# Performance work log

Measured on AMD Instinct MI355X. Metric: run time of the kernel, lower is better.

The kernel has to match this reference:

```python
import jax, jax.numpy as jnp
import numpy as np

N_NODES = 50000
N_EDGES = 800000
IN_CH = 128
H1, C1 = 2, 64            # gat1: heads=2, out=64 -> concat 128
H2, C2 = 1, 32            # gat2: heads=1, out=out_channels=32, concat=False
NEG_SLOPE = 0.2           # PyG GATConv default negative_slope


def setup_inputs() -> dict:
    key = jax.random.key(0)
    ks = jax.random.split(key, 12)
    s = 0.05
    return {
        "x": jax.random.normal(ks[0], (N_NODES, IN_CH), dtype=jnp.float32),
        "edge_index": jax.random.randint(ks[1], (2, N_EDGES), 0, N_NODES, dtype=jnp.int64),
        # layer 1 params
        "W1": jax.random.normal(ks[2], (IN_CH, H1 * C1), dtype=jnp.float32) * s,
        "a1_src": jax.random.normal(ks[3], (H1, C1), dtype=jnp.float32) * s,
        "a1_dst": jax.random.normal(ks[4], (H1, C1), dtype=jnp.float32) * s,
        "b1": jax.random.normal(ks[5], (H1 * C1,), dtype=jnp.float32) * s,
        # layer 2 params
        "W2": jax.random.normal(ks[6], (H1 * C1, H2 * C2), dtype=jnp.float32) * s,
        "a2_src": jax.random.normal(ks[7], (H2, C2), dtype=jnp.float32) * s,
        "a2_dst": jax.random.normal(ks[8], (H2, C2), dtype=jnp.float32) * s,
        "b2": jax.random.normal(ks[9], (C2,), dtype=jnp.float32) * s,
    }


def _gat_conv(x, src, dst, W, a_src, a_dst, b, heads, out_ch, concat):
    """PyG GATConv (eval mode, self-loops already in src/dst)."""
    n = x.shape[0]
    h = (x @ W).reshape(n, heads, out_ch)               # [N,H,C]
    s_src = jnp.sum(h * a_src, axis=-1)                  # [N,H]
    s_dst = jnp.sum(h * a_dst, axis=-1)                  # [N,H]
    e = jax.nn.leaky_relu(s_src[src] + s_dst[dst], NEG_SLOPE)   # [E,H]
    # segment softmax over incoming edges of each destination node
    emax = jax.ops.segment_max(e, dst, num_segments=n)   # [N,H]
    emax = jax.lax.stop_gradient(emax)
    ee = jnp.exp(e - emax[dst])
    den = jax.ops.segment_sum(ee, dst, num_segments=n)   # [N,H]
    alpha = ee / den[dst]                                # [E,H]
    out = jax.ops.segment_sum(h[src] * alpha[..., None], dst, num_segments=n)  # [N,H,C]
    out = out.reshape(n, heads * out_ch) if concat else out.mean(axis=1)
    return out + b


def reference(x, edge_index, W1, a1_src, a1_dst, b1, W2, a2_src, a2_dst, b2):
    n = x.shape[0]
    loops = jnp.arange(n, dtype=edge_index.dtype)
    src = jnp.concatenate([edge_index[0], loops])
    dst = jnp.concatenate([edge_index[1], loops])
    h = _gat_conv(x, src, dst, W1, a1_src, a1_dst, b1, H1, C1, concat=True)
    h = jax.nn.elu(h)
    out = _gat_conv(h, src, dst, W2, a2_src, a2_dst, b2, H2, C2, concat=False)
    return out
```

## Files before the change

kernel.cpp:

```cpp
#include <hip/hip_runtime.h>
#include <math.h>

#define N_NODES 50000
#define N_EDGES 800000
#define E_TOT   (N_EDGES + N_NODES)
#define SCAN_BLK 1024
#define SCAN_NB  ((N_NODES + SCAN_BLK - 1) / SCAN_BLK)

__device__ __forceinline__ float bcast_f(float v, int srclane) {
    return __uint_as_float(__builtin_amdgcn_readlane(__float_as_uint(v), srclane));
}

__global__ __launch_bounds__(128) void gemm1_tiled(
    const float* __restrict__ x, const float* __restrict__ W,
    const float* __restrict__ a_src, const float* __restrict__ a_dst,
    float* __restrict__ h, float* __restrict__ s_src, float* __restrict__ s_dst)
{
    __shared__ float xs[64][68];
    __shared__ float wt[64][68];
    const int tid  = threadIdx.x;
    const int colT = tid & 15;
    const int rowT = tid >> 4;
    const int half = blockIdx.x & 1;
    const int r0   = (blockIdx.x >> 1) * 64;
    const int c0   = half * 64;

    float acc[4][8];
    #pragma unroll
    for (int j = 0; j < 4; ++j)
        #pragma unroll
        for (int i = 0; i < 8; ++i) acc[j][i] = 0.f;

    for (int kc = 0; kc < 2; ++kc) {
        const int kbase = kc * 64;
        #pragma unroll
        for (int it = 0; it < 8; ++it) {
            int q = it * 128 + tid;
            int row = q >> 4, k4 = q & 15;
            float4 v = make_float4(0.f, 0.f, 0.f, 0.f);
            if (r0 + row < N_NODES)
                v = *(const float4*)&x[(size_t)(r0 + row) * 128 + kbase + k4 * 4];
            *(float4*)&xs[row][k4 * 4] = v;
        }
        #pragma unroll
        for (int it = 0; it < 8; ++it) {
            int q = it * 128 + tid;
            int c = q & 63, k4 = q >> 6;
            float4 v;
            v.x = W[(kbase + k4 * 4 + 0) * 128 + c0 + c];
            v.y = W[(kbase + k4 * 4 + 1) * 128 + c0 + c];
            v.z = W[(kbase + k4 * 4 + 2) * 128 + c0 + c];
            v.w = W[(kbase + k4 * 4 + 3) * 128 + c0 + c];
            *(float4*)&wt[c][k4 * 4] = v;
        }
        __syncthreads();
        #pragma unroll 4
        for (int k4 = 0; k4 < 16; ++k4) {
            float4 wv[4], xv[8];
            #pragma unroll
            for (int j = 0; j < 4; ++j) wv[j] = *(const float4*)&wt[colT + 16 * j][k4 * 4];
            #pragma unroll
            for (int i = 0; i < 8; ++i) xv[i] = *(const float4*)&xs[rowT + 8 * i][k4 * 4];
            #pragma unroll
            for (int j = 0; j < 4; ++j)
                #pragma unroll
                for (int i = 0; i < 8; ++i)
                    acc[j][i] += wv[j].x * xv[i].x + wv[j].y * xv[i].y
                               + wv[j].z * xv[i].z + wv[j].w * xv[i].w;
        }
        __syncthreads();
    }

    #pragma unroll
    for (int i = 0; i < 8; ++i) {
        const int row = r0 + rowT + 8 * i;
        float vs = 0.f, vd = 0.f;
        #pragma unroll
        for (int j = 0; j < 4; ++j) {
            const int c = c0 + colT + 16 * j;
            const float a = acc[j][i];
            vs += a * a_src[c];
            vd += a * a_dst[c];
            if (row < N_NODES) h[(size_t)row * 128 + c] = a;
        }
        #pragma unroll
        for (int off = 8; off >= 1; off >>= 1) {
            vs += __shfl_xor(vs, off, 64);
            vd += __shfl_xor(vd, off, 64);
        }
        if (colT == 0 && row < N_NODES) {
            s_src[row * 2 + half] = vs;
            s_dst[row * 2 + half] = vd;
        }
    }
}

__global__ __launch_bounds__(128) void gemm2_tiled(
    const float* __restrict__ h2, const float* __restrict__ W,
    const float* __restrict__ a_src, const float* __restrict__ a_dst,
    float* __restrict__ g, float* __restrict__ s_src, float* __restrict__ s_dst)
{
    __shared__ float xs[128][68];
    __shared__ float wt[32][68];
    const int tid  = threadIdx.x;
    const int colT = tid & 7;
    const int rowT = tid >> 3;
    const int r0   = blockIdx.x * 128;

    float acc[4][8];
    #pragma unroll
    for (int j = 0; j < 4; ++j)
        #pragma unroll
        for (int i = 0; i < 8; ++i) acc[j][i] = 0.f;

    for (int kc = 0; kc < 2; ++kc) {
        const int kbase = kc * 64;
        #pragma unroll
        for (int it = 0; it < 16; ++it) {
            int q = it * 128 + tid;
            int row = q >> 4, k4 = q & 15;
            float4 v = make_float4(0.f, 0.f, 0.f, 0.f);
            if (r0 + row < N_NODES)
                v = *(const float4*)&h2[(size_t)(r0 + row) * 128 + kbase + k4 * 4];
            *(float4*)&xs[row][k4 * 4] = v;
        }
        #pragma unroll
        for (int it = 0; it < 4; ++it) {
            int q = it * 128 + tid;
            int c = q & 31, k4 = q >> 5;
            float4 v;
            v.x = W[(kbase + k4 * 4 + 0) * 32 + c];
            v.y = W[(kbase + k4 * 4 + 1) * 32 + c];
            v.z = W[(kbase + k4 * 4 + 2) * 32 + c];
            v.w = W[(kbase + k4 * 4 + 3) * 32 + c];
            *(float4*)&wt[c][k4 * 4] = v;
        }
        __syncthreads();
        #pragma unroll 4
        for (int k4 = 0; k4 < 16; ++k4) {
            float4 wv[4], xv[8];
            #pragma unroll
            for (int j = 0; j < 4; ++j) wv[j] = *(const float4*)&wt[colT + 8 * j][k4 * 4];
            #pragma unroll
            for (int i = 0; i < 8; ++i) xv[i] = *(const float4*)&xs[rowT + 16 * i][k4 * 4];
            #pragma unroll
            for (int j = 0; j < 4; ++j)
                #pragma unroll
                for (int i = 0; i < 8; ++i)
                    acc[j][i] += wv[j].x * xv[i].x + wv[j].y * xv[i].y
                               + wv[j].z * xv[i].z + wv[j].w * xv[i].w;
        }
        __syncthreads();
    }

    #pragma unroll
    for (int i = 0; i < 8; ++i) {
        const int row = r0 + rowT + 16 * i;
        float vs = 0.f, vd = 0.f;
        #pragma unroll
        for (int j = 0; j < 4; ++j) {
            const int c = colT + 8 * j;
            const float a = acc[j][i];
            vs += a * a_src[c];
            vd += a * a_dst[c];
            if (row < N_NODES) g[(size_t)row * 32 + c] = a;
        }
        #pragma unroll
        for (int off = 4; off >= 1; off >>= 1) {
            vs += __shfl_xor(vs, off, 64);
            vd += __shfl_xor(vd, off, 64);
        }
        if (colT == 0 && row < N_NODES) {
            s_src[row] = vs;
            s_dst[row] = vd;
        }
    }
}

__global__ void hist_kernel(const int* __restrict__ edst, int* __restrict__ deg)
{
    int e = blockIdx.x * blockDim.x + threadIdx.x;
    if (e >= E_TOT) return;
    int d = (e < N_EDGES) ? edst[e] : (e - N_EDGES);
    atomicAdd(&deg[d], 1);
}

__global__ __launch_bounds__(1024) void scanA_kernel(
    const int* __restrict__ deg, int* __restrict__ locscan, int* __restrict__ partial)
{
    __shared__ int buf[SCAN_BLK];
    const int t = threadIdx.x;
    const int i = blockIdx.x * SCAN_BLK + t;
    int v = (i < N_NODES) ? deg[i] : 0;
    buf[t] = v;
    __syncthreads();
    #pragma unroll
    for (int off = 1; off < SCAN_BLK; off <<= 1) {
        int xx = (t >= off) ? buf[t - off] : 0;
        __syncthreads();
        buf[t] += xx;
        __syncthreads();
    }
    if (i < N_NODES) locscan[i] = buf[t] - v;
    if (t == SCAN_BLK - 1) partial[blockIdx.x] = buf[t];
}

__global__ void scanB_kernel(int* __restrict__ partial)
{
    const int t = threadIdx.x;
    int orig = (t < SCAN_NB) ? partial[t] : 0;
    int v = orig;
    #pragma unroll
    for (int off = 1; off < 64; off <<= 1) {
        int xx = __shfl_up(v, off, 64);
        if (t >= off) v += xx;
    }
    if (t < SCAN_NB) partial[t] = v - orig;
}

__global__ void scanC_kernel(const int* __restrict__ locscan, const int* __restrict__ partial,
                             int* __restrict__ offsets, int* __restrict__ cursor)
{
    int i = blockIdx.x * 256 + threadIdx.x;
    if (i >= N_NODES) return;
    int o = locscan[i] + partial[i >> 10];
    offsets[i] = o;
    cursor[i]  = o;
    if (i == 0) offsets[N_NODES] = E_TOT;
}

__global__ void scatter_kernel(const int* __restrict__ esrc, const int* __restrict__ edst,
                               int* __restrict__ cursor, int* __restrict__ csr_src)
{
    int e = blockIdx.x * blockDim.x + threadIdx.x;
    if (e >= E_TOT) return;
    int s, d;
    if (e < N_EDGES) { s = esrc[e]; d = edst[e]; } else { s = d = e - N_EDGES; }
    int pos = atomicAdd(&cursor[d], 1);
    csr_src[pos] = s;
}

__global__ __launch_bounds__(256) void fused_agg1_kernel(
    const int* __restrict__ csr_src, const int* __restrict__ offsets,
    const float* __restrict__ s_src, const float* __restrict__ s_dst,
    const float* __restrict__ h, const float* __restrict__ b,
    float* __restrict__ h2)
{
    const int wid  = threadIdx.x >> 6;
    const int lane = threadIdx.x & 63;
    const int d = blockIdx.x * 4 + wid;
    if (d >= N_NODES) return;
    const int beg = offsets[d], end = offsets[d + 1];
    const float sd0 = s_dst[d * 2], sd1 = s_dst[d * 2 + 1];
    float m0 = -1e30f, m1 = -1e30f;
    float den0 = 0.f, den1 = 0.f, acc0 = 0.f, acc1 = 0.f;

    for (int pos = beg; pos < end; pos += 64) {
        const int n = min(64, end - pos);
        int s = 0;
        float v0 = -1e30f, v1 = -1e30f;
        if (lane < n) {
            s = csr_src[pos + lane];
            const float2 ss = *(const float2*)&s_src[s * 2];
            v0 = ss.x + sd0;  v0 = v0 > 0.f ? v0 : 0.2f * v0;
            v1 = ss.y + sd1;  v1 = v1 > 0.f ? v1 : 0.2f * v1;
        }
        float cm0 = v0, cm1 = v1;
        #pragma unroll
        for (int off = 32; off >= 1; off >>= 1) {
            cm0 = fmaxf(cm0, __shfl_xor(cm0, off, 64));
            cm1 = fmaxf(cm1, __shfl_xor(cm1, off, 64));
        }
        const float nm0 = fmaxf(m0, cm0), nm1 = fmaxf(m1, cm1);
        const float sc0 = __expf(m0 - nm0), sc1 = __expf(m1 - nm1);
        acc0 *= sc0; den0 *= sc0;
        acc1 *= sc1; den1 *= sc1;
        m0 = nm0; m1 = nm1;
        const float e0 = (lane < n) ? __expf(v0 - nm0) : 0.f;
        const float e1 = (lane < n) ? __expf(v1 - nm1) : 0.f;
        float t0 = e0, t1 = e1;
        #pragma unroll
        for (int off = 32; off >= 1; off >>= 1) {
            t0 += __shfl_xor(t0, off, 64);
            t1 += __shfl_xor(t1, off, 64);
        }
        den0 += t0; den1 += t1;
        for (int i = 0; i < n; ++i) {
            const int   si = __builtin_amdgcn_readlane(s, i);
            const float a0 = bcast_f(e0, i);
            const float a1 = bcast_f(e1, i);
            const float* hp = h + (size_t)si * 128;
            acc0 += a0 * hp[lane];
            acc1 += a1 * hp[64 + lane];
        }
    }
    float o0 = acc0 / den0 + b[lane];
    float o1 = acc1 / den1 + b[64 + lane];
    o0 = o0 > 0.f ? o0 : expm1f(o0);
    o1 = o1 > 0.f ? o1 : expm1f(o1);
    h2[d * 128 + lane]      = o0;
    h2[d * 128 + 64 + lane] = o1;
}

__global__ __launch_bounds__(256) void fused_agg2_kernel(
    const int* __restrict__ csr_src, const int* __restrict__ offsets,
    const float* __restrict__ s_src, const float* __restrict__ s_dst,
    const float* __restrict__ g, const float* __restrict__ b,
    float* __restrict__ out)
{
    const int grp      = threadIdx.x >> 5;
    const int lane     = threadIdx.x & 31;
    const int halfbase = threadIdx.x & 32;
    const int d = blockIdx.x * 8 + grp;
    if (d >= N_NODES) return;
    const int beg = offsets[d], end = offsets[d + 1];
    const float sd = s_dst[d];
    float m = -1e30f, den = 0.f, acc = 0.f;

    for (int pos = beg; pos < end; pos += 32) {
        const int n = min(32, end - pos);
        int s = 0;
        float v = -1e30f;
        if (lane < n) {
            s = csr_src[pos + lane];
            v = s_src[s] + sd;  v = v > 0.f ? v : 0.2f * v;
        }
        float cm = v;
        #pragma unroll
        for (int off = 16; off >= 1; off >>= 1)
            cm = fmaxf(cm, __shfl_xor(cm, off, 32));
        const float nm = fmaxf(m, cm);
        const float sc = __expf(m - nm);
        acc *= sc; den *= sc;
        m = nm;
        const float e = (lane < n) ? __expf(v - nm) : 0.f;
        float t = e;
        #pragma unroll
        for (int off = 16; off >= 1; off >>= 1)
            t += __shfl_xor(t, off, 32);
        den += t;
        for (int i = 0; i < n; ++i) {
            const int   si = __shfl(s, i + halfbase, 64);
            const float a  = __shfl(e, i + halfbase, 64);
            acc += a * g[(size_t)si * 32 + lane];
        }
    }
    out[d * 32 + lane] = acc / den + b[lane];
}

extern "C" void kernel_launch(void* const* d_in, const int* in_sizes, int n_in,
                              void* d_out, int out_size, void* d_ws, size_t ws_size,
                              hipStream_t stream)
{
    const float* x   = (const float*)d_in[0];
    const int*   ei  = (const int*)d_in[1];
    const float* W1  = (const float*)d_in[2];
    const float* a1s = (const float*)d_in[3];
    const float* a1d = (const float*)d_in[4];
    const float* b1  = (const float*)d_in[5];
    const float* W2  = (const float*)d_in[6];
    const float* a2s = (const float*)d_in[7];
    const float* a2d = (const float*)d_in[8];
    const float* b2  = (const float*)d_in[9];
    float* out = (float*)d_out;

    const int* esrc = ei;
    const int* edst = ei + N_EDGES;

    float* ws = (float*)d_ws;
    float* h1  = ws;
    float* h2  = h1  + (size_t)N_NODES * 128;
    float* s1s = h2  + (size_t)N_NODES * 128;
    float* s1d = s1s + 2 * N_NODES;
    float* s2s = s1d + 2 * N_NODES;
    float* s2d = s2s + N_NODES;
    int* deg     = (int*)(s2d + N_NODES);
    int* offsets = deg + N_NODES;
    int* cursor  = offsets + N_NODES + 1;
    int* csr_src = cursor + N_NODES;
    int* locscan = csr_src + E_TOT;
    int* partial = locscan + N_NODES;
    float* g2 = h1;

    hipMemsetAsync(deg, 0, (size_t)N_NODES * 4, stream);
    hist_kernel<<<(E_TOT + 255) / 256, 256, 0, stream>>>(edst, deg);
    scanA_kernel<<<SCAN_NB, SCAN_BLK, 0, stream>>>(deg, locscan, partial);
    scanB_kernel<<<1, 64, 0, stream>>>(partial);
    scanC_kernel<<<(N_NODES + 255) / 256, 256, 0, stream>>>(locscan, partial, offsets, cursor);
    scatter_kernel<<<(E_TOT + 255) / 256, 256, 0, stream>>>(esrc, edst, cursor, csr_src);

    gemm1_tiled<<<((N_NODES + 63) / 64) * 2, 128, 0, stream>>>(x, W1, a1s, a1d, h1, s1s, s1d);
    fused_agg1_kernel<<<(N_NODES + 3) / 4, 256, 0, stream>>>(
        csr_src, offsets, s1s, s1d, h1, b1, h2);

    gemm2_tiled<<<(N_NODES + 127) / 128, 128, 0, stream>>>(h2, W2, a2s, a2d, g2, s2s, s2d);
    fused_agg2_kernel<<<(N_NODES + 7) / 8, 256, 0, stream>>>(
        csr_src, offsets, s2s, s2d, g2, b2, out);
}
```

Measured before the change: 292.9 us.

## Vectorize GAT aggregation gathers with float4 and process multiple edges per wave

Both aggregation kernels now read neighbor feature rows as float4 instead of scalar loads. In layer 1 each wave handles two edges per step, one per half-wave. In layer 2 each 32-lane group handles four edges per step. The next row's load is issued before the current FMAs, to hide gather latency. Partial accumulators are combined with cross-lane shuffles at the end, and fewer lanes write the output. The goal is fewer load instructions and more memory-level parallelism in latency-bound neighbor gathers, at the cost of extra shuffles and some lane-select logic.

```diff
diff --git a/kernel.cpp b/kernel.cpp
--- a/kernel.cpp
+++ b/kernel.cpp
@@ -248,12 +248,16 @@
 {
     const int wid  = threadIdx.x >> 6;
     const int lane = threadIdx.x & 63;
+    const int q    = lane & 31;
+    const bool odd    = lane >= 32;
+    const bool headhi = q >= 16;
     const int d = blockIdx.x * 4 + wid;
     if (d >= N_NODES) return;
     const int beg = offsets[d], end = offsets[d + 1];
     const float sd0 = s_dst[d * 2], sd1 = s_dst[d * 2 + 1];
     float m0 = -1e30f, m1 = -1e30f;
-    float den0 = 0.f, den1 = 0.f, acc0 = 0.f, acc1 = 0.f;
+    float den0 = 0.f, den1 = 0.f;
+    float4 acc = make_float4(0.f, 0.f, 0.f, 0.f);
 
     for (int pos = beg; pos < end; pos += 64) {
         const int n = min(64, end - pos);
@@ -273,8 +277,9 @@
         }
         const float nm0 = fmaxf(m0, cm0), nm1 = fmaxf(m1, cm1);
         const float sc0 = __expf(m0 - nm0), sc1 = __expf(m1 - nm1);
-        acc0 *= sc0; den0 *= sc0;
-        acc1 *= sc1; den1 *= sc1;
+        den0 *= sc0; den1 *= sc1;
+        const float asc = headhi ? sc1 : sc0;
+        acc.x *= asc; acc.y *= asc; acc.z *= asc; acc.w *= asc;
         m0 = nm0; m1 = nm1;
         const float e0 = (lane < n) ? __expf(v0 - nm0) : 0.f;
         const float e1 = (lane < n) ? __expf(v1 - nm1) : 0.f;
@@ -285,21 +290,47 @@
             t1 += __shfl_xor(t1, off, 64);
         }
         den0 += t0; den1 += t1;
-        for (int i = 0; i < n; ++i) {
-            const int   si = __builtin_amdgcn_readlane(s, i);
-            const float a0 = bcast_f(e0, i);
-            const float a1 = bcast_f(e1, i);
-            const float* hp = h + (size_t)si * 128;
-            acc0 += a0 * hp[lane];
-            acc1 += a1 * hp[64 + lane];
-        }
-    }
-    float o0 = acc0 / den0 + b[lane];
-    float o1 = acc1 / den1 + b[64 + lane];
-    o0 = o0 > 0.f ? o0 : expm1f(o0);
-    o1 = o1 > 0.f ? o1 : expm1f(o1);
-    h2[d * 128 + lane]      = o0;
-    h2[d * 128 + 64 + lane] = o1;
+
+        const int steps = (n + 1) >> 1;
+        int sia = __builtin_amdgcn_readlane(s, 0);
+        int sib = __builtin_amdgcn_readlane(s, 1);
+        int si  = odd ? sib : sia;
+        float4 hv = *(const float4*)&h[(size_t)si * 128 + q * 4];
+        for (int i = 0; i < steps; ++i) {
+            const float e0a = bcast_f(e0, 2 * i),     e1a = bcast_f(e1, 2 * i);
+            const float e0b = bcast_f(e0, 2 * i + 1), e1b = bcast_f(e1, 2 * i + 1);
+            const float a = headhi ? (odd ? e1b : e1a) : (odd ? e0b : e0a);
+            const float4 cur = hv;
+            if (i + 1 < steps) {
+                const int na = __builtin_amdgcn_readlane(s, 2 * i + 2);
+                const int nb = __builtin_amdgcn_readlane(s, 2 * i + 3);
+                si = odd ? nb : na;
+                hv = *(const float4*)&h[(size_t)si * 128 + q * 4];
+            }
+            acc.x += a * cur.x;
+            acc.y += a * cur.y;
+            acc.z += a * cur.z;
+            acc.w += a * cur.w;
+        }
+    }
+    acc.x += __shfl_xor(acc.x, 32, 64);
+    acc.y += __shfl_xor(acc.y, 32, 64);
+    acc.z += __shfl_xor(acc.z, 32, 64);
+    acc.w += __shfl_xor(acc.w, 32, 64);
+    if (lane < 32) {
+        const float den = headhi ? den1 : den0;
+        const float4 b4 = *(const float4*)&b[q * 4];
+        float4 o;
+        o.x = acc.x / den + b4.x;
+        o.y = acc.y / den + b4.y;
+        o.z = acc.z / den + b4.z;
+        o.w = acc.w / den + b4.w;
+        o.x = o.x > 0.f ? o.x : expm1f(o.x);
+        o.y = o.y > 0.f ? o.y : expm1f(o.y);
+        o.z = o.z > 0.f ? o.z : expm1f(o.z);
+        o.w = o.w > 0.f ? o.w : expm1f(o.w);
+        *(float4*)&h2[(size_t)d * 128 + q * 4] = o;
+    }
 }
 
 __global__ __launch_bounds__(256) void fused_agg2_kernel(
@@ -309,20 +340,23 @@
     float* __restrict__ out)
 {
     const int grp      = threadIdx.x >> 5;
-    const int lane     = threadIdx.x & 31;
+    const int q        = threadIdx.x & 31;
     const int halfbase = threadIdx.x & 32;
+    const int slot     = q >> 3;
+    const int r        = q & 7;
     const int d = blockIdx.x * 8 + grp;
     if (d >= N_NODES) return;
     const int beg = offsets[d], end = offsets[d + 1];
     const float sd = s_dst[d];
-    float m = -1e30f, den = 0.f, acc = 0.f;
+    float m = -1e30f, den = 0.f;
+    float4 acc = make_float4(0.f, 0.f, 0.f, 0.f);
 
     for (int pos = beg; pos < end; pos += 32) {
         const int n = min(32, end - pos);
         int s = 0;
         float v = -1e30f;
-        if (lane < n) {
-            s = csr_src[pos + lane];
+        if (q < n) {
+            s = csr_src[pos + q];
             v = s_src[s] + sd;  v = v > 0.f ? v : 0.2f * v;
         }
         float cm = v;
@@ -331,21 +365,45 @@
             cm = fmaxf(cm, __shfl_xor(cm, off, 32));
         const float nm = fmaxf(m, cm);
         const float sc = __expf(m - nm);
-        acc *= sc; den *= sc;
+        den *= sc;
+        acc.x *= sc; acc.y *= sc; acc.z *= sc; acc.w *= sc;
         m = nm;
-        const float e = (lane < n) ? __expf(v - nm) : 0.f;
+        const float e = (q < n) ? __expf(v - nm) : 0.f;
         float t = e;
         #pragma unroll
         for (int off = 16; off >= 1; off >>= 1)
             t += __shfl_xor(t, off, 32);
         den += t;
-        for (int i = 0; i < n; ++i) {
-            const int   si = __shfl(s, i + halfbase, 64);
-            const float a  = __shfl(e, i + halfbase, 64);
-            acc += a * g[(size_t)si * 32 + lane];
-        }
-    }
-    out[d * 32 + lane] = acc / den + b[lane];
+
+        const int steps = (n + 3) >> 2;
+        int src0 = halfbase + min(slot, 31);
+        int si = __shfl(s, src0, 64);
+        float4 gv = *(const float4*)&g[(size_t)si * 32 + r * 4];
+        for (int i = 0; i < steps; ++i) {
+            const float a = __shfl(e, halfbase + min(4 * i + slot, 31), 64);
+            const float4 cur = gv;
+            const int jn = halfbase + min(4 * (i + 1) + slot, 31);
+            si = __shfl(s, jn, 64);
+            gv = *(const float4*)&g[(size_t)si * 32 + r * 4];
+            acc.x += a * cur.x;
+            acc.y += a * cur.y;
+            acc.z += a * cur.z;
+            acc.w += a * cur.w;
+        }
+    }
+    acc.x += __shfl_xor(acc.x, 8, 32);  acc.y += __shfl_xor(acc.y, 8, 32);
+    acc.z += __shfl_xor(acc.z, 8, 32);  acc.w += __shfl_xor(acc.w, 8, 32);
+    acc.x += __shfl_xor(acc.x, 16, 32); acc.y += __shfl_xor(acc.y, 16, 32);
+    acc.z += __shfl_xor(acc.z, 16, 32); acc.w += __shfl_xor(acc.w, 16, 32);
+    if (slot == 0) {
+        const float4 b4 = *(const float4*)&b[r * 4];
+        float4 o;
+        o.x = acc.x / den + b4.x;
+        o.y = acc.y / den + b4.y;
+        o.z = acc.z / den + b4.z;
+        o.w = acc.w / den + b4.w;
+        *(float4*)&out[(size_t)d * 32 + r * 4] = o;
+    }
 }
 
 extern "C" void kernel_launch(void* const* d_in, const int* in_sizes, int n_in,
```

Measured after the change: 264.4 us. -9.7%, faster.

## Store projected features in fp16 and gather with vectorized multi-edge lanes

Applied to the files above, without the earlier changes.

The GEMM outputs h1 and g2 are now stored as half precision, which halves the bytes each aggregation kernel gathers per edge. The aggregation kernels are restructured so each lane loads 16 bytes (8 halves) per edge and several edges are processed in parallel across lane slots. The next edge's features are prefetched while the current one accumulates, and partial sums are reduced across slots with shuffles at the end. This trades fp16 rounding of intermediate features, plus some extra shuffle and register cost, for much lower gather bandwidth and fewer serialized iterations.

```diff
diff --git a/kernel.cpp b/kernel.cpp
--- a/kernel.cpp
+++ b/kernel.cpp
@@ -1,4 +1,5 @@
 #include <hip/hip_runtime.h>
+#include <hip/hip_fp16.h>
 #include <math.h>
 
 #define N_NODES 50000
@@ -7,14 +8,10 @@
 #define SCAN_BLK 1024
 #define SCAN_NB  ((N_NODES + SCAN_BLK - 1) / SCAN_BLK)
 
-__device__ __forceinline__ float bcast_f(float v, int srclane) {
-    return __uint_as_float(__builtin_amdgcn_readlane(__float_as_uint(v), srclane));
-}
-
 __global__ __launch_bounds__(128) void gemm1_tiled(
     const float* __restrict__ x, const float* __restrict__ W,
     const float* __restrict__ a_src, const float* __restrict__ a_dst,
-    float* __restrict__ h, float* __restrict__ s_src, float* __restrict__ s_dst)
+    __half* __restrict__ h, float* __restrict__ s_src, float* __restrict__ s_dst)
 {
     __shared__ float xs[64][68];
     __shared__ float wt[64][68];
@@ -81,7 +78,7 @@
             const float a = acc[j][i];
             vs += a * a_src[c];
             vd += a * a_dst[c];
-            if (row < N_NODES) h[(size_t)row * 128 + c] = a;
+            if (row < N_NODES) h[(size_t)row * 128 + c] = __float2half(a);
         }
         #pragma unroll
         for (int off = 8; off >= 1; off >>= 1) {
@@ -98,7 +95,7 @@
 __global__ __launch_bounds__(128) void gemm2_tiled(
     const float* __restrict__ h2, const float* __restrict__ W,
     const float* __restrict__ a_src, const float* __restrict__ a_dst,
-    float* __restrict__ g, float* __restrict__ s_src, float* __restrict__ s_dst)
+    __half* __restrict__ g, float* __restrict__ s_src, float* __restrict__ s_dst)
 {
     __shared__ float xs[128][68];
     __shared__ float wt[32][68];
@@ -163,7 +160,7 @@
             const float a = acc[j][i];
             vs += a * a_src[c];
             vd += a * a_dst[c];
-            if (row < N_NODES) g[(size_t)row * 32 + c] = a;
+            if (row < N_NODES) g[(size_t)row * 32 + c] = __float2half(a);
         }
         #pragma unroll
         for (int off = 4; off >= 1; off >>= 1) {
@@ -243,17 +240,23 @@
 __global__ __launch_bounds__(256) void fused_agg1_kernel(
     const int* __restrict__ csr_src, const int* __restrict__ offsets,
     const float* __restrict__ s_src, const float* __restrict__ s_dst,
-    const float* __restrict__ h, const float* __restrict__ b,
+    const __half* __restrict__ h, const float* __restrict__ b,
     float* __restrict__ h2)
 {
     const int wid  = threadIdx.x >> 6;
     const int lane = threadIdx.x & 63;
+    const int p    = lane & 15;
+    const int slot = lane >> 4;
+    const bool headhi = p >= 8;
     const int d = blockIdx.x * 4 + wid;
     if (d >= N_NODES) return;
     const int beg = offsets[d], end = offsets[d + 1];
     const float sd0 = s_dst[d * 2], sd1 = s_dst[d * 2 + 1];
     float m0 = -1e30f, m1 = -1e30f;
-    float den0 = 0.f, den1 = 0.f, acc0 = 0.f, acc1 = 0.f;
+    float den0 = 0.f, den1 = 0.f;
+    float acc[8];
+    #pragma unroll
+    for (int k = 0; k < 8; ++k) acc[k] = 0.f;
 
     for (int pos = beg; pos < end; pos += 64) {
         const int n = min(64, end - pos);
@@ -273,8 +276,10 @@
         }
         const float nm0 = fmaxf(m0, cm0), nm1 = fmaxf(m1, cm1);
         const float sc0 = __expf(m0 - nm0), sc1 = __expf(m1 - nm1);
-        acc0 *= sc0; den0 *= sc0;
-        acc1 *= sc1; den1 *= sc1;
+        den0 *= sc0; den1 *= sc1;
+        const float asc = headhi ? sc1 : sc0;
+        #pragma unroll
+        for (int k = 0; k < 8; ++k) acc[k] *= asc;
         m0 = nm0; m1 = nm1;
         const float e0 = (lane < n) ? __expf(v0 - nm0) : 0.f;
         const float e1 = (lane < n) ? __expf(v1 - nm1) : 0.f;
@@ -285,44 +290,78 @@
             t1 += __shfl_xor(t1, off, 64);
         }
         den0 += t0; den1 += t1;
-        for (int i = 0; i < n; ++i) {
-            const int   si = __builtin_amdgcn_readlane(s, i);
-            const float a0 = bcast_f(e0, i);
-            const float a1 = bcast_f(e1, i);
-            const float* hp = h + (size_t)si * 128;
-            acc0 += a0 * hp[lane];
-            acc1 += a1 * hp[64 + lane];
-        }
-    }
-    float o0 = acc0 / den0 + b[lane];
-    float o1 = acc1 / den1 + b[64 + lane];
-    o0 = o0 > 0.f ? o0 : expm1f(o0);
-    o1 = o1 > 0.f ? o1 : expm1f(o1);
-    h2[d * 128 + lane]      = o0;
-    h2[d * 128 + 64 + lane] = o1;
+
+        const int steps = (n + 3) >> 2;
+        int j  = slot;
+        int si = __shfl(s, j, 64);
+        float4 raw = *(const float4*)&h[(size_t)si * 128 + p * 8];
+        float av0 = __shfl(e0, j, 64);
+        float av1 = __shfl(e1, j, 64);
+        float av  = headhi ? av1 : av0;
+        for (int i = 0; i < steps; ++i) {
+            const float4 cur = raw;
+            const float  ac  = av;
+            if (i + 1 < steps) {
+                j   = 4 * (i + 1) + slot;
+                si  = __shfl(s, j, 64);
+                raw = *(const float4*)&h[(size_t)si * 128 + p * 8];
+                av0 = __shfl(e0, j, 64);
+                av1 = __shfl(e1, j, 64);
+                av  = headhi ? av1 : av0;
+            }
+            const __half2* hp = (const __half2*)&cur;
+            #pragma unroll
+            for (int k = 0; k < 4; ++k) {
+                const float2 f = __half22float2(hp[k]);
+                acc[2 * k]     += ac * f.x;
+                acc[2 * k + 1] += ac * f.y;
+            }
+        }
+    }
+    #pragma unroll
+    for (int k = 0; k < 8; ++k) {
+        acc[k] += __shfl_xor(acc[k], 16, 64);
+        acc[k] += __shfl_xor(acc[k], 32, 64);
+    }
+    if (slot == 0) {
+        const float den = headhi ? den1 : den0;
+        float o[8];
+        #pragma unroll
+        for (int k = 0; k < 8; ++k) {
+            o[k] = acc[k] / den + b[p * 8 + k];
+            o[k] = o[k] > 0.f ? o[k] : expm1f(o[k]);
+        }
+        *(float4*)&h2[(size_t)d * 128 + p * 8]     = make_float4(o[0], o[1], o[2], o[3]);
+        *(float4*)&h2[(size_t)d * 128 + p * 8 + 4] = make_float4(o[4], o[5], o[6], o[7]);
+    }
 }
 
 __global__ __launch_bounds__(256) void fused_agg2_kernel(
     const int* __restrict__ csr_src, const int* __restrict__ offsets,
     const float* __restrict__ s_src, const float* __restrict__ s_dst,
-    const float* __restrict__ g, const float* __restrict__ b,
+    const __half* __restrict__ g, const float* __restrict__ b,
     float* __restrict__ out)
 {
     const int grp      = threadIdx.x >> 5;
-    const int lane     = threadIdx.x & 31;
+    const int q        = threadIdx.x & 31;
     const int halfbase = threadIdx.x & 32;
+    const int p2       = q & 3;
+    const int slot2    = q >> 2;
     const int d = blockIdx.x * 8 + grp;
     if (d >= N_NODES) return;
     const int beg = offsets[d], end = offsets[d + 1];
     const float sd = s_dst[d];
-    float m = -1e30f, den = 0.f, acc = 0.f;
+    float m = -1e30f, den = 0.f;
+    float acc[8];
+    #pragma unroll
+    for (int k = 0; k < 8; ++k) acc[k] = 0.f;
 
     for (int pos = beg; pos < end; pos += 32) {
         const int n = min(32, end - pos);
         int s = 0;
         float v = -1e30f;
-        if (lane < n) {
-            s = csr_src[pos + lane];
+        if (q < n) {
+            s = csr_src[pos + q];
             v = s_src[s] + sd;  v = v > 0.f ? v : 0.2f * v;
         }
         float cm = v;
@@ -331,21 +370,54 @@
             cm = fmaxf(cm, __shfl_xor(cm, off, 32));
         const float nm = fmaxf(m, cm);
         const float sc = __expf(m - nm);
-        acc *= sc; den *= sc;
+        den *= sc;
+        #pragma unroll
+        for (int k = 0; k < 8; ++k) acc[k] *= sc;
         m = nm;
-        const float e = (lane < n) ? __expf(v - nm) : 0.f;
+        const float e = (q < n) ? __expf(v - nm) : 0.f;
         float t = e;
         #pragma unroll
         for (int off = 16; off >= 1; off >>= 1)
             t += __shfl_xor(t, off, 32);
         den += t;
-        for (int i = 0; i < n; ++i) {
-            const int   si = __shfl(s, i + halfbase, 64);
-            const float a  = __shfl(e, i + halfbase, 64);
-            acc += a * g[(size_t)si * 32 + lane];
-        }
-    }
-    out[d * 32 + lane] = acc / den + b[lane];
+
+        const int steps = (n + 7) >> 3;
+        int j  = slot2;
+        int si = __shfl(s, halfbase + j, 64);
+        float4 raw = *(const float4*)&g[(size_t)si * 32 + p2 * 8];
+        float av = __shfl(e, halfbase + j, 64);
+        for (int i = 0; i < steps; ++i) {
+            const float4 cur = raw;
+            const float  ac  = av;
+            if (i + 1 < steps) {
+                j  = 8 * (i + 1) + slot2;
+                si = __shfl(s, halfbase + j, 64);
+                raw = *(const float4*)&g[(size_t)si * 32 + p2 * 8];
+                av  = __shfl(e, halfbase + j, 64);
+            }
+            const __half2* gp = (const __half2*)&cur;
+            #pragma unroll
+            for (int k = 0; k < 4; ++k) {
+                const float2 f = __half22float2(gp[k]);
+                acc[2 * k]     += ac * f.x;
+                acc[2 * k + 1] += ac * f.y;
+            }
+        }
+    }
+    #pragma unroll
+    for (int k = 0; k < 8; ++k) {
+        acc[k] += __shfl_xor(acc[k], 4, 32);
+        acc[k] += __shfl_xor(acc[k], 8, 32);
+        acc[k] += __shfl_xor(acc[k], 16, 32);
+    }
+    if (slot2 == 0) {
+        float o[8];
+        #pragma unroll
+        for (int k = 0; k < 8; ++k)
+            o[k] = acc[k] / den + b[p2 * 8 + k];
+        *(float4*)&out[(size_t)d * 32 + p2 * 8]     = make_float4(o[0], o[1], o[2], o[3]);
+        *(float4*)&out[(size_t)d * 32 + p2 * 8 + 4] = make_float4(o[4], o[5], o[6], o[7]);
+    }
 }
 
 extern "C" void kernel_launch(void* const* d_in, const int* in_sizes, int n_in,
@@ -368,8 +440,8 @@
     const int* edst = ei + N_EDGES;
 
     float* ws = (float*)d_ws;
-    float* h1  = ws;
-    float* h2  = h1  + (size_t)N_NODES * 128;
+    __half* h1 = (__half*)ws;
+    float* h2  = ws  + (size_t)N_NODES * 128;
     float* s1s = h2  + (size_t)N_NODES * 128;
     float* s1d = s1s + 2 * N_NODES;
     float* s2s = s1d + 2 * N_NODES;
@@ -380,7 +452,7 @@
     int* csr_src = cursor + N_NODES;
     int* locscan = csr_src + E_TOT;
     int* partial = locscan + N_NODES;
-    float* g2 = h1;
+    __half* g2 = (__half*)ws;
 
     hipMemsetAsync(deg, 0, (size_t)N_NODES * 4, stream);
     hist_kernel<<<(E_TOT + 255) / 256, 256, 0, stream>>>(edst, deg);
```

New measurement: 249.9 us. 14.7% less time.
